# Performance work log

Measured on AMD Instinct MI355X. Metric: run time of the kernel, lower is better.

The kernel has to match this reference:

```python
import jax, jax.numpy as jnp
import numpy as np


def setup_inputs() -> dict:
    key = jax.random.key(0)
    ks = jax.random.split(key, 12)
    B, T, N, H = 32, 128, 256, 512
    s = 0.05
    return {
        "data": jax.random.normal(ks[0], (B, T, N), jnp.float32),
        "h0": jax.random.normal(ks[1], (B, H), jnp.float32),
        "gru_kernel": jax.random.normal(ks[2], (N, 3 * H), jnp.float32) * s,
        "gru_rkernel": jax.random.normal(ks[3], (H, 3 * H), jnp.float32) * s,
        "gru_bias": jax.random.normal(ks[4], (2, 3 * H), jnp.float32) * s,  # (input_bias, recurrent_bias), reset_after=True
        "w1_w": jax.random.normal(ks[5], (T, T), jnp.float32) * s,
        "w1_b": jax.random.normal(ks[6], (T,), jnp.float32) * s,
        "w2_w": jax.random.normal(ks[7], (H, T), jnp.float32) * s,
        "w2_b": jax.random.normal(ks[8], (T,), jnp.float32) * s,
        "v_w": jax.random.normal(ks[9], (T, 1), jnp.float32) * s,
        "v_b": jax.random.normal(ks[10], (1,), jnp.float32) * s,
        "n": N,
    }


def reference(data, h0, gru_kernel, gru_rkernel, gru_bias, w1_w, w1_b, w2_w, w2_b, v_w, v_b, n):
    B, T, N = data.shape
    b_in, b_rec = gru_bias[0], gru_bias[1]

    # Keras GRUCell (reset_after=True, gate order z,r,h)
    def step(h, x_t):
        mx = x_t @ gru_kernel + b_in          # (B,3H)
        mh = h @ gru_rkernel + b_rec          # (B,3H)
        xz, xr, xh = jnp.split(mx, 3, axis=-1)
        hz, hr, hh = jnp.split(mh, 3, axis=-1)
        z = jax.nn.sigmoid(xz + hz)
        r = jax.nn.sigmoid(xr + hr)
        c = jnp.tanh(xh + r * hh)
        h_new = z * h + (1.0 - z) * c
        return h_new, h_new

    xs = jnp.swapaxes(data, 0, 1)                               # (T,B,N)
    _, hs = jax.lax.scan(step, h0, xs)                          # (T,B,H) hidden state after each step

    # Input attention, vectorized over t (attention does not feed back into the GRU)
    x_perm = jnp.swapaxes(data, 1, 2)                           # (B,N,T)
    score_x = jnp.einsum('bnt,tu->bnu', x_perm, w1_w) + w1_b    # (B,N,T), constant across steps
    h_proj = hs @ w2_w + w2_b                                   # (T,B,T)
    e = jnp.tanh(score_x[None, :, :, :] + h_proj[:, :, None, :])  # (T,B,N,T)
    score = jnp.einsum('tbnu,u->tbn', e, v_w[:, 0]) + v_b[0]    # (T,B,N)
    alpha = jax.nn.softmax(score, axis=-1)                      # (T,B,N) softmax over features

    # Replicates tf.reshape(alpha_seq.stack(), (-1, T, n)) on (T,B,1,N) (row-major)
    alpha_seq = alpha.reshape(-1, T, N)                         # (B,T,N) via flat reindex, as in original
    return data * alpha_seq
```

## Files before the change

kernel.cpp:

```cpp
#include <hip/hip_runtime.h>
#include <math.h>

#define BB 32
#define TT 128
#define NF 256
#define HH 512
#define G3 1536
#define NWG 64

__device__ __forceinline__ float sigmoidf_(float x) { return 1.f / (1.f + __expf(-x)); }
__device__ __forceinline__ float tanh_fast(float x) {
    float e = __expf(2.f * x);
    return 1.f - 2.f / (e + 1.f);
}
__device__ __forceinline__ float sel4_(float a0, float a1, float a2, float a3, int s) {
    float s01 = (s & 1) ? a1 : a0;
    float s23 = (s & 1) ? a3 : a2;
    return (s & 2) ? s23 : s01;
}

__global__ __launch_bounds__(256) void k_hinit(const float* __restrict__ h0,
                                               float* __restrict__ hg2) {
    int idx = blockIdx.x * 256 + threadIdx.x;
    int i = idx & 511, b = idx >> 9;
    hg2[i * BB + b] = h0[b * HH + i];
}

__global__ __launch_bounds__(256) void k_pack(const float* __restrict__ rk,
                                              float4* __restrict__ rk4) {
    int gidx = blockIdx.x * 256 + threadIdx.x;
    int wg = gidx >> 12;
    int idx = gidx & 4095;
    int k = idx >> 3, s = idx & 7;
    int jjL = s ^ (((k >> 7) & 3) << 1);
    const float* r = rk + (size_t)k * G3 + wg * 8 + jjL;
    rk4[gidx] = make_float4(r[0], r[512], r[1024], 0.f);
}

__global__ __launch_bounds__(256) void k_mx(const float* __restrict__ data,
                                            const float* __restrict__ gk,
                                            const float* __restrict__ bias_in,
                                            float* __restrict__ mxT) {
    __shared__ __align__(16) float xs[NF * 8];
    int bx = blockIdx.x;
    int t = bx >> 2, b0 = (bx & 3) * 8;
    int tid = threadIdx.x;
    for (int idx = tid; idx < 8 * NF; idx += 256) {
        int bb = idx >> 8, k = idx & 255;
        xs[k * 8 + bb] = data[((size_t)(b0 + bb) * TT + t) * NF + k];
    }
    __syncthreads();
    float acc[6][8];
#pragma unroll
    for (int jj = 0; jj < 6; jj++)
#pragma unroll
        for (int bb = 0; bb < 8; bb++) acc[jj][bb] = 0.f;

    for (int k = 0; k < NF; k++) {
        float4 xa = *(const float4*)&xs[k * 8];
        float4 xb = *(const float4*)&xs[k * 8 + 4];
        float xv[8] = {xa.x, xa.y, xa.z, xa.w, xb.x, xb.y, xb.z, xb.w};
#pragma unroll
        for (int jj = 0; jj < 6; jj++) {
            float g = gk[(size_t)k * G3 + jj * 256 + tid];
#pragma unroll
            for (int bb = 0; bb < 8; bb++) acc[jj][bb] += g * xv[bb];
        }
    }
#pragma unroll
    for (int jj = 0; jj < 6; jj++) {
        int j = jj * 256 + tid;
        float bi = bias_in[j];
#pragma unroll
        for (int bb = 0; bb < 8; bb++)
            mxT[((size_t)t * G3 + j) * BB + b0 + bb] = acc[jj][bb] + bi;
    }
}

extern __shared__ float4 wl4_dyn[];

__global__ __launch_bounds__(256, 1) void k_gstep(const float4* __restrict__ rk4,
                                                  const float* __restrict__ gbias,
                                                  const float* __restrict__ mxT,
                                                  float* __restrict__ hg2,
                                                  float* __restrict__ hs,
                                                  int t) {
    __shared__ __align__(16) float4 h4[HH * 8];
    const int tid = threadIdx.x;
    const int wg  = blockIdx.x;
    const int jj  = tid >> 5;
    const int bq  = (tid >> 2) & 7;
    const int ks  = tid & 3;
    const int i0  = wg * 8;
    const int i   = i0 + jj;
    const int batch = bq * 4 + ks;
    const int jjs = jj ^ (ks << 1);
    const int bqs = bq ^ (ks << 1);

    {
        const float4* src = rk4 + (size_t)wg * 4096;
#pragma unroll
        for (int it = 0; it < 16; it++) {
            int idx = it * 256 + tid;
            wl4_dyn[idx] = src[idx];
        }
    }
    {
        const float4* hgr = (const float4*)(hg2 + (t & 1) * (HH * BB));
#pragma unroll
        for (int it = 0; it < 16; it++) {
            int idx = it * 256 + tid;
            h4[idx] = hgr[idx ^ ((((idx >> 10) & 3)) << 1)];
        }
    }
    const float* brec = gbias + G3;
    const float bz = brec[i], br_ = brec[512 + i], bh = brec[1024 + i];
    __syncthreads();

    const float* mxc = mxT + (size_t)t * G3 * BB;
    float mz = mxc[(size_t)i * BB + batch];
    float mr = mxc[(size_t)(512 + i) * BB + batch];
    float mh = mxc[(size_t)(1024 + i) * BB + batch];

    float az0 = 0.f, az1 = 0.f, az2 = 0.f, az3 = 0.f;
    float ar0 = 0.f, ar1 = 0.f, ar2 = 0.f, ar3 = 0.f;
    float ah0 = 0.f, ah1 = 0.f, ah2 = 0.f, ah3 = 0.f;
    const float4* wp  = wl4_dyn + ks * 1024 + jjs;
    const float4* hp2 = &h4[ks * 1024 + bqs];
#pragma unroll 4
    for (int kk = 0; kk < 128; kk++) {
        float4 w = wp[kk * 8];
        float4 h = hp2[kk * 8];
        az0 += w.x * h.x; az1 += w.x * h.y; az2 += w.x * h.z; az3 += w.x * h.w;
        ar0 += w.y * h.x; ar1 += w.y * h.y; ar2 += w.y * h.z; ar3 += w.y * h.w;
        ah0 += w.z * h.x; ah1 += w.z * h.y; ah2 += w.z * h.z; ah3 += w.z * h.w;
    }

    az0 += __shfl_xor(az0, 1); az1 += __shfl_xor(az1, 1);
    az2 += __shfl_xor(az2, 1); az3 += __shfl_xor(az3, 1);
    ar0 += __shfl_xor(ar0, 1); ar1 += __shfl_xor(ar1, 1);
    ar2 += __shfl_xor(ar2, 1); ar3 += __shfl_xor(ar3, 1);
    ah0 += __shfl_xor(ah0, 1); ah1 += __shfl_xor(ah1, 1);
    ah2 += __shfl_xor(ah2, 1); ah3 += __shfl_xor(ah3, 1);
    az0 += __shfl_xor(az0, 2); az1 += __shfl_xor(az1, 2);
    az2 += __shfl_xor(az2, 2); az3 += __shfl_xor(az3, 2);
    ar0 += __shfl_xor(ar0, 2); ar1 += __shfl_xor(ar1, 2);
    ar2 += __shfl_xor(ar2, 2); ar3 += __shfl_xor(ar3, 2);
    ah0 += __shfl_xor(ah0, 2); ah1 += __shfl_xor(ah1, 2);
    ah2 += __shfl_xor(ah2, 2); ah3 += __shfl_xor(ah3, 2);

    float azt = sel4_(az0, az1, az2, az3, ks);
    float art = sel4_(ar0, ar1, ar2, ar3, ks);
    float aht = sel4_(ah0, ah1, ah2, ah3, ks);

    float z = sigmoidf_(mz + azt + bz);
    float r = sigmoidf_(mr + art + br_);
    float c = tanhf(mh + r * (aht + bh));
    float hold = ((const float*)&h4[i * 8 + (bq ^ ((((i >> 7) & 3)) << 1))])[ks];
    float hn = z * hold + (1.f - z) * c;

    hg2[((t + 1) & 1) * (HH * BB) + i * BB + batch] = hn;

    __syncthreads();
    float* hstage = (float*)wl4_dyn;
    hstage[jj * 36 + batch] = hn;
    __syncthreads();
    {
        int b2 = tid >> 3, ii = tid & 7;
        hs[((size_t)t * BB + b2) * HH + i0 + ii] = hstage[ii * 36 + b2];
    }
}

__global__ __launch_bounds__(256) void k_sx(const float* __restrict__ data,
                                            const float* __restrict__ w1,
                                            const float* __restrict__ w1b,
                                            float* __restrict__ sx) {
    int bx = blockIdx.x;
    int b = bx >> 4, ug = bx & 15;
    int n = threadIdx.x;
    float acc[8] = {0, 0, 0, 0, 0, 0, 0, 0};
    const float* dp = data + (size_t)b * TT * NF + n;
    for (int t = 0; t < TT; t++) {
        float x = dp[(size_t)t * NF];
#pragma unroll
        for (int uu = 0; uu < 8; uu++) acc[uu] += x * w1[t * TT + ug * 8 + uu];
    }
#pragma unroll
    for (int uu = 0; uu < 8; uu++) {
        int u = ug * 8 + uu;
        sx[((size_t)b * TT + u) * NF + n] = acc[uu] + w1b[u];
    }
}

__global__ __launch_bounds__(256) void k_hp(const float* __restrict__ hs,
                                            const float* __restrict__ w2,
                                            const float* __restrict__ w2b,
                                            float* __restrict__ hp) {
    __shared__ float hsl[8 * HH];
    int r0 = blockIdx.x * 8;
    int tid = threadIdx.x;
    for (int idx = tid; idx < 8 * HH; idx += 256)
        hsl[idx] = hs[(size_t)r0 * HH + idx];
    __syncthreads();
    int u = tid & 127, rh = tid >> 7;
    float acc[4] = {0, 0, 0, 0};
    for (int k = 0; k < HH; k++) {
        float w = w2[k * TT + u];
#pragma unroll
        for (int rr = 0; rr < 4; rr++) acc[rr] += hsl[(rh * 4 + rr) * HH + k] * w;
    }
    float wb = w2b[u];
#pragma unroll
    for (int rr = 0; rr < 4; rr++)
        hp[(size_t)(r0 + rh * 4 + rr) * TT + u] = acc[rr] + wb;
}

__global__ __launch_bounds__(256) void k_attn(const float* __restrict__ data,
                                              const float* __restrict__ sx,
                                              const float* __restrict__ hp,
                                              const float* __restrict__ v_w,
                                              const float* __restrict__ v_b,
                                              float* __restrict__ out) {
    __shared__ float hv[TT];
    __shared__ float vv[TT];
    __shared__ float red[8];
    int r = blockIdx.x;
    int b = r & 31;
    int n = threadIdx.x;
    if (n < TT) {
        hv[n] = hp[(size_t)r * TT + n];
        vv[n] = v_w[n];
    }
    __syncthreads();
    float s = v_b[0];
    const float* sxp = sx + (size_t)b * TT * NF + n;
    for (int u = 0; u < TT; u++) {
        float e = tanh_fast(sxp[(size_t)u * NF] + hv[u]);
        s += vv[u] * e;
    }
    float m = s;
#pragma unroll
    for (int off = 32; off >= 1; off >>= 1) m = fmaxf(m, __shfl_xor(m, off));
    int lane = n & 63, wid = n >> 6;
    if (lane == 0) red[wid] = m;
    __syncthreads();
    float bm = fmaxf(fmaxf(red[0], red[1]), fmaxf(red[2], red[3]));
    float p = __expf(s - bm);
    float ps = p;
#pragma unroll
    for (int off = 32; off >= 1; off >>= 1) ps += __shfl_xor(ps, off);
    if (lane == 0) red[4 + wid] = ps;
    __syncthreads();
    float denom = red[4] + red[5] + red[6] + red[7];
    float alpha = p / denom;
    size_t idx = (size_t)r * NF + n;
    out[idx] = data[idx] * alpha;
}

extern "C" void kernel_launch(void* const* d_in, const int* in_sizes, int n_in,
                              void* d_out, int out_size, void* d_ws, size_t ws_size,
                              hipStream_t stream) {
    const float* data = (const float*)d_in[0];
    const float* h0   = (const float*)d_in[1];
    const float* gk   = (const float*)d_in[2];
    const float* rk   = (const float*)d_in[3];
    const float* gb   = (const float*)d_in[4];
    const float* w1   = (const float*)d_in[5];
    const float* w1b  = (const float*)d_in[6];
    const float* w2   = (const float*)d_in[7];
    const float* w2b  = (const float*)d_in[8];
    const float* vw   = (const float*)d_in[9];
    const float* vb   = (const float*)d_in[10];
    float* out = (float*)d_out;

    float* ws  = (float*)d_ws;
    float* mxT = ws;
    float* hs  = mxT + 6291456;
    float* sxb = hs + 2097152;
    float* hpb = sxb + 1048576;
    float* hg2 = hpb + 524288;
    float4* rk4 = (float4*)(hg2 + 32768);

    k_hinit<<<64, 256, 0, stream>>>(h0, hg2);
    k_pack<<<1024, 256, 0, stream>>>(rk, rk4);
    k_mx<<<512, 256, 0, stream>>>(data, gk, gb, mxT);

    for (int t = 0; t < TT; t++)
        k_gstep<<<NWG, 256, 65536, stream>>>(rk4, gb, mxT, hg2, hs, t);

    k_sx<<<512, 256, 0, stream>>>(data, w1, w1b, sxb);
    k_hp<<<512, 256, 0, stream>>>(hs, w2, w2b, hpb);
    k_attn<<<4096, 256, 0, stream>>>(data, sxb, hpb, vw, vb, out);
}
```

Before: 1.278 ms.

## Rework GRU step: 8-way k-split, direct global-to-LDS loads, fast rcp tanh

The per-timestep GRU kernel now splits the reduction dimension eight ways instead of four, and each thread accumulates 8 batches per gate, with a matching XOR swizzle of the hidden-state tile and a three-level shuffle reduction. The weight and hidden-state tiles are copied into LDS with gfx950 global_load_lds 16-byte transfers instead of staging through registers. The aim is to cut per-step latency in the serial recurrence, which runs once per timestep. Separately, the attention tanh uses a hardware reciprocal, and its inner loop is unrolled. This raises register pressure and depends on __syncthreads waiting for the asynchronous LDS loads.

```diff
diff --git a/kernel.cpp b/kernel.cpp
--- a/kernel.cpp
+++ b/kernel.cpp
@@ -11,12 +11,17 @@
 __device__ __forceinline__ float sigmoidf_(float x) { return 1.f / (1.f + __expf(-x)); }
 __device__ __forceinline__ float tanh_fast(float x) {
     float e = __expf(2.f * x);
-    return 1.f - 2.f / (e + 1.f);
-}
-__device__ __forceinline__ float sel4_(float a0, float a1, float a2, float a3, int s) {
-    float s01 = (s & 1) ? a1 : a0;
-    float s23 = (s & 1) ? a3 : a2;
-    return (s & 2) ? s23 : s01;
+    return 1.f - 2.f * __builtin_amdgcn_rcpf(e + 1.f);
+}
+__device__ __forceinline__ float sel8_(float a0, float a1, float a2, float a3,
+                                       float a4, float a5, float a6, float a7, int s) {
+    float x0 = (s & 1) ? a1 : a0;
+    float x1 = (s & 1) ? a3 : a2;
+    float x2 = (s & 1) ? a5 : a4;
+    float x3 = (s & 1) ? a7 : a6;
+    float y0 = (s & 2) ? x1 : x0;
+    float y1 = (s & 2) ? x3 : x2;
+    return (s & 4) ? y1 : y0;
 }
 
 __global__ __launch_bounds__(256) void k_hinit(const float* __restrict__ h0,
@@ -89,20 +94,20 @@
     const int tid = threadIdx.x;
     const int wg  = blockIdx.x;
     const int jj  = tid >> 5;
-    const int bq  = (tid >> 2) & 7;
-    const int ks  = tid & 3;
+    const int bqp = (tid >> 3) & 3;
+    const int ks  = tid & 7;
     const int i0  = wg * 8;
     const int i   = i0 + jj;
-    const int batch = bq * 4 + ks;
-    const int jjs = jj ^ (ks << 1);
-    const int bqs = bq ^ (ks << 1);
+    const int batch = bqp * 8 + ks;
 
     {
         const float4* src = rk4 + (size_t)wg * 4096;
 #pragma unroll
         for (int it = 0; it < 16; it++) {
             int idx = it * 256 + tid;
-            wl4_dyn[idx] = src[idx];
+            __builtin_amdgcn_global_load_lds(
+                (const __attribute__((address_space(1))) void*)(src + idx),
+                (__attribute__((address_space(3))) void*)&wl4_dyn[idx], 16, 0, 0);
         }
     }
     {
@@ -110,7 +115,10 @@
 #pragma unroll
         for (int it = 0; it < 16; it++) {
             int idx = it * 256 + tid;
-            h4[idx] = hgr[idx ^ ((((idx >> 10) & 3)) << 1)];
+            int sidx = (idx & ~7) | ((idx & 7) ^ ((idx >> 9) & 7));
+            __builtin_amdgcn_global_load_lds(
+                (const __attribute__((address_space(1))) void*)(hgr + sidx),
+                (__attribute__((address_space(3))) void*)&h4[idx], 16, 0, 0);
         }
     }
     const float* brec = gbias + G3;
@@ -122,41 +130,45 @@
     float mr = mxc[(size_t)(512 + i) * BB + batch];
     float mh = mxc[(size_t)(1024 + i) * BB + batch];
 
-    float az0 = 0.f, az1 = 0.f, az2 = 0.f, az3 = 0.f;
-    float ar0 = 0.f, ar1 = 0.f, ar2 = 0.f, ar3 = 0.f;
-    float ah0 = 0.f, ah1 = 0.f, ah2 = 0.f, ah3 = 0.f;
-    const float4* wp  = wl4_dyn + ks * 1024 + jjs;
-    const float4* hp2 = &h4[ks * 1024 + bqs];
+    float az[8], ar[8], ah[8];
+#pragma unroll
+    for (int e = 0; e < 8; e++) { az[e] = 0.f; ar[e] = 0.f; ah[e] = 0.f; }
+
+    const float4* wp  = wl4_dyn + (size_t)ks * 512 + (jj ^ (((ks >> 1) & 3) << 1));
+    const float4* hpA = h4 + (size_t)ks * 512 + ((bqp << 1) ^ ks);
+    const float4* hpB = h4 + (size_t)ks * 512 + (((bqp << 1) | 1) ^ ks);
 #pragma unroll 4
-    for (int kk = 0; kk < 128; kk++) {
-        float4 w = wp[kk * 8];
-        float4 h = hp2[kk * 8];
-        az0 += w.x * h.x; az1 += w.x * h.y; az2 += w.x * h.z; az3 += w.x * h.w;
-        ar0 += w.y * h.x; ar1 += w.y * h.y; ar2 += w.y * h.z; ar3 += w.y * h.w;
-        ah0 += w.z * h.x; ah1 += w.z * h.y; ah2 += w.z * h.z; ah3 += w.z * h.w;
-    }
-
-    az0 += __shfl_xor(az0, 1); az1 += __shfl_xor(az1, 1);
-    az2 += __shfl_xor(az2, 1); az3 += __shfl_xor(az3, 1);
-    ar0 += __shfl_xor(ar0, 1); ar1 += __shfl_xor(ar1, 1);
-    ar2 += __shfl_xor(ar2, 1); ar3 += __shfl_xor(ar3, 1);
-    ah0 += __shfl_xor(ah0, 1); ah1 += __shfl_xor(ah1, 1);
-    ah2 += __shfl_xor(ah2, 1); ah3 += __shfl_xor(ah3, 1);
-    az0 += __shfl_xor(az0, 2); az1 += __shfl_xor(az1, 2);
-    az2 += __shfl_xor(az2, 2); az3 += __shfl_xor(az3, 2);
-    ar0 += __shfl_xor(ar0, 2); ar1 += __shfl_xor(ar1, 2);
-    ar2 += __shfl_xor(ar2, 2); ar3 += __shfl_xor(ar3, 2);
-    ah0 += __shfl_xor(ah0, 2); ah1 += __shfl_xor(ah1, 2);
-    ah2 += __shfl_xor(ah2, 2); ah3 += __shfl_xor(ah3, 2);
-
-    float azt = sel4_(az0, az1, az2, az3, ks);
-    float art = sel4_(ar0, ar1, ar2, ar3, ks);
-    float aht = sel4_(ah0, ah1, ah2, ah3, ks);
+    for (int kk = 0; kk < 64; kk++) {
+        float4 w  = wp[kk * 8];
+        float4 ha = hpA[kk * 8];
+        float4 hb = hpB[kk * 8];
+        az[0] += w.x * ha.x; az[1] += w.x * ha.y; az[2] += w.x * ha.z; az[3] += w.x * ha.w;
+        az[4] += w.x * hb.x; az[5] += w.x * hb.y; az[6] += w.x * hb.z; az[7] += w.x * hb.w;
+        ar[0] += w.y * ha.x; ar[1] += w.y * ha.y; ar[2] += w.y * ha.z; ar[3] += w.y * ha.w;
+        ar[4] += w.y * hb.x; ar[5] += w.y * hb.y; ar[6] += w.y * hb.z; ar[7] += w.y * hb.w;
+        ah[0] += w.z * ha.x; ah[1] += w.z * ha.y; ah[2] += w.z * ha.z; ah[3] += w.z * ha.w;
+        ah[4] += w.z * hb.x; ah[5] += w.z * hb.y; ah[6] += w.z * hb.z; ah[7] += w.z * hb.w;
+    }
+
+#pragma unroll
+    for (int m = 1; m <= 4; m <<= 1) {
+#pragma unroll
+        for (int e = 0; e < 8; e++) {
+            az[e] += __shfl_xor(az[e], m);
+            ar[e] += __shfl_xor(ar[e], m);
+            ah[e] += __shfl_xor(ah[e], m);
+        }
+    }
+
+    float azt = sel8_(az[0], az[1], az[2], az[3], az[4], az[5], az[6], az[7], ks);
+    float art = sel8_(ar[0], ar[1], ar[2], ar[3], ar[4], ar[5], ar[6], ar[7], ks);
+    float aht = sel8_(ah[0], ah[1], ah[2], ah[3], ah[4], ah[5], ah[6], ah[7], ks);
 
     float z = sigmoidf_(mz + azt + bz);
     float r = sigmoidf_(mr + art + br_);
     float c = tanhf(mh + r * (aht + bh));
-    float hold = ((const float*)&h4[i * 8 + (bq ^ ((((i >> 7) & 3)) << 1))])[ks];
+    int hq = ((bqp << 1) + (ks >> 2)) ^ ((i >> 6) & 7);
+    float hold = ((const float*)&h4[(size_t)i * 8 + hq])[ks & 3];
     float hn = z * hold + (1.f - z) * c;
 
     hg2[((t + 1) & 1) * (HH * BB) + i * BB + batch] = hn;
@@ -234,6 +246,7 @@
     __syncthreads();
     float s = v_b[0];
     const float* sxp = sx + (size_t)b * TT * NF + n;
+#pragma unroll 4
     for (int u = 0; u < TT; u++) {
         float e = tanh_fast(sxp[(size_t)u * NF] + hv[u]);
         s += vv[u] * e;
```

New measurement: 1.268 ms. No clear change (-0.7%).
